# Kernel tuning notes

Hardware: AMD Instinct MI355X
Metric: run time of the kernel (lower is better)

Reference implementation:

```python
import jax, jax.numpy as jnp
import numpy as np

NUM_HEADS = 8

def mha(q, k, v, in_w, in_b, out_w, out_b):
    # q:[B,Lq,E] k,v:[B,Lk,E]; torch nn.MultiheadAttention math (batch_first)
    B, Lq, E = q.shape
    Lk = k.shape[1]
    H = NUM_HEADS
    D = E // H
    wq, wk, wv = in_w[:E], in_w[E:2*E], in_w[2*E:]      # each [E,E], torch layout [out,in]
    bq, bk, bv = in_b[:E], in_b[E:2*E], in_b[2*E:]
    qp = (q @ wq.T + bq).reshape(B, Lq, H, D)
    kp = (k @ wk.T + bk).reshape(B, Lk, H, D)
    vp = (v @ wv.T + bv).reshape(B, Lk, H, D)
    scores = jnp.einsum('bqhd,bkhd->bhqk', qp, kp) / jnp.sqrt(jnp.asarray(D, q.dtype))
    attn = jax.nn.softmax(scores, axis=-1)
    ctx = jnp.einsum('bhqk,bkhd->bqhd', attn, vp).reshape(B, Lq, E)
    return ctx @ out_w.T + out_b

def setup_inputs() -> dict:
    key = jax.random.key(0)
    ks = jax.random.split(key, 12)
    B, IN, E, M, NB = 2048, 1024, 512, 256, 8
    s = lambda *d: 1.0 / np.sqrt(d[-1])
    return {
        'x':      jax.random.normal(ks[0], (B, IN), jnp.float32),
        'memory': jax.random.uniform(ks[1], (M, E), jnp.float32, -s(E), s(E)),
        'enc_w':  jax.random.uniform(ks[2], (E, IN), jnp.float32, -s(IN), s(IN)),
        'enc_b':  jnp.zeros((E,), jnp.float32),
        'blk_w':  jax.random.uniform(ks[3], (NB, E, E), jnp.float32, -s(E), s(E)),
        'blk_b':  jnp.zeros((NB, E), jnp.float32),
        'in_w':   jax.random.uniform(ks[4], (3 * E, E), jnp.float32, -s(E), s(E)),
        'in_b':   jnp.zeros((3 * E,), jnp.float32),
        'out_w':  jax.random.uniform(ks[5], (E, E), jnp.float32, -s(E), s(E)),
        'out_b':  jnp.zeros((E,), jnp.float32),
        'dec_w':  jax.random.uniform(ks[6], (IN, E), jnp.float32, -s(E), s(E)),
        'dec_b':  jnp.zeros((IN,), jnp.float32),
    }

def reference(x, memory, enc_w, enc_b, blk_w, blk_b, in_w, in_b, out_w, out_b, dec_w, dec_b):
    B = x.shape[0]
    encoded = jnp.tanh(x @ enc_w.T + enc_b)                     # [B,E]
    # all block linears at once: [B, NB, E]
    memory_updates = jnp.einsum('be,noe->bno', encoded, blk_w) + blk_b
    mem = jnp.broadcast_to(memory[None], (B,) + memory.shape)   # [B,M,E]
    attended = mha(memory_updates, mem, mem, in_w, in_b, out_w, out_b)
    updated_memory = mem + jnp.mean(attended, axis=1, keepdims=True)
    retrieved = mha(encoded[:, None, :], updated_memory, updated_memory, in_w, in_b, out_w, out_b)
    output = retrieved[:, 0, :] @ dec_w.T + dec_b               # [B,IN]
    return output, updated_memory
```

## Files before the change

### kernel.cpp

```cpp
#include <hip/hip_runtime.h>
#include <math.h>


typedef __attribute__((ext_vector_type(8))) short short8;
typedef __attribute__((ext_vector_type(4))) float f32x4;
typedef unsigned short u16;

#define GLOAD16(gp, lp)                                                        \
    __builtin_amdgcn_global_load_lds(                                          \
        (const __attribute__((address_space(1))) void*)(gp),                   \
        (__attribute__((address_space(3))) void*)(lp), 16, 0, 0)

__device__ inline u16 bf16_rn(float x) {
    unsigned u = __float_as_uint(x);
    unsigned r = (u + 0x7FFFu + ((u >> 16) & 1u)) >> 16;
    return (u16)r;
}
__device__ inline float bf16_f(u16 h) { return __uint_as_float(((unsigned)h) << 16); }

__global__ __launch_bounds__(256)
void prep_all(const float* __restrict__ x, const float* __restrict__ mm,
              const float* __restrict__ ew, const float* __restrict__ iw,
              const float* __restrict__ ow, const float* __restrict__ dw,
              const float* __restrict__ blk_w,
              const float* __restrict__ in_b, const float* __restrict__ blk_b,
              const float* __restrict__ out_b, const float* __restrict__ dec_b,
              u16* __restrict__ xh, u16* __restrict__ xl,
              u16* __restrict__ mh, u16* __restrict__ ml,
              u16* __restrict__ ewh, u16* __restrict__ ewl,
              u16* __restrict__ iwh, u16* __restrict__ iwl,
              u16* __restrict__ owh, u16* __restrict__ owl,
              u16* __restrict__ dwh, u16* __restrict__ dwl,
              u16* __restrict__ bwTh, u16* __restrict__ bwTl,
              u16* __restrict__ owTh, u16* __restrict__ owTl,
              float* __restrict__ bias1, float* __restrict__ bias2,
              float* __restrict__ bias_uv)
{
    __shared__ float T[32][33];
    const int id = blockIdx.x;
    const int t = threadIdx.x;
    if (id < 2304) {
        const int z = id >> 8, within = id & 255;
        const float* s; u16 *dh, *dl;
        if (z < 8) { s = blk_w + (long long)z * 262144;
                     dh = bwTh + (long long)z * 262144; dl = bwTl + (long long)z * 262144; }
        else       { s = ow; dh = owTh; dl = owTl; }
        const int c0 = (within & 15) * 32, r0 = (within >> 4) * 32;
        const int tx = t & 31, ty = t >> 5;
        #pragma unroll
        for (int rr = 0; rr < 4; ++rr)
            T[ty + rr * 8][tx] = s[(long long)(r0 + ty + rr * 8) * 512 + c0 + tx];
        __syncthreads();
        #pragma unroll
        for (int rr = 0; rr < 4; ++rr) {
            float v = T[tx][ty + rr * 8];
            long long o = (long long)(c0 + ty + rr * 8) * 512 + r0 + tx;
            u16 hh = bf16_rn(v);
            dh[o] = hh; dl[o] = bf16_rn(v - bf16_f(hh));
        }
    } else if (id < 2326) {
        int idx = (id - 2304) * 256 + t;
        if (idx < 4096) {
            int n = idx >> 9, f = idx & 511;
            const float* wr_ = iw + (long long)f * 512;
            const float* bb  = blk_b + n * 512;
            float s = in_b[f];
            for (int o = 0; o < 512; ++o) s += wr_[o] * bb[o];
            bias1[idx] = s;
        } else if (idx < 5120) {
            int i = idx - 4096;
            const float* dr = dw + (long long)i * 512;
            float s = dec_b[i];
            for (int f = 0; f < 512; ++f) s += dr[f] * out_b[f];
            bias2[i] = s;
        } else if (idx < 5632) {
            int f = idx - 5120;
            const float* wv = iw + (long long)(1024 + f) * 512;
            float s = 0.f;
            for (int e = 0; e < 512; ++e) s += wv[e] * out_b[e];
            bias_uv[f] = s;
        }
    } else {
        const long long total = 1081344;
        const long long stride = 2048LL * 256;
        for (long long i = (long long)(id - 2326) * 256 + t; i < total; i += stride) {
            const float* src; u16 *hi, *lo; long long j;
            if (i < 524288)      { src = x;  hi = xh;  lo = xl;  j = i; }
            else if (i < 557056) { src = mm; hi = mh;  lo = ml;  j = i - 524288; }
            else if (i < 688128) { src = ew; hi = ewh; lo = ewl; j = i - 557056; }
            else if (i < 884736) { src = iw; hi = iwh; lo = iwl; j = i - 688128; }
            else if (i < 950272) { src = ow; hi = owh; lo = owl; j = i - 884736; }
            else                 { src = dw; hi = dwh; lo = dwl; j = i - 950272; }
            float4 v = reinterpret_cast<const float4*>(src)[j];
            u16 h0 = bf16_rn(v.x), h1 = bf16_rn(v.y), h2 = bf16_rn(v.z), h3 = bf16_rn(v.w);
            ushort4 hv = {h0, h1, h2, h3};
            ushort4 lv = {bf16_rn(v.x - bf16_f(h0)), bf16_rn(v.y - bf16_f(h1)),
                          bf16_rn(v.z - bf16_f(h2)), bf16_rn(v.w - bf16_f(h3))};
            reinterpret_cast<ushort4*>(hi)[j] = hv;
            reinterpret_cast<ushort4*>(lo)[j] = lv;
        }
    }
}

struct ZD {
    const u16 *Ah, *Al, *Bh, *Bl;
    const float* bias;
    float* Cf; u16 *Ch, *Cl;
    int M, lda, ldb, ldc, K, act, omode;
    float scale;
};
template<int NZ> struct ZPack { ZD d[NZ]; };

__device__ __forceinline__ void gemm_zd(const ZD& dz, int m0, int n0,
    u16 (*Ash)[32], u16 (*Asl)[32], u16 (*Bsh)[32], u16 (*Bsl)[32])
{
    const int t  = threadIdx.x;
    const int lane = t & 63;
    const int wid  = t >> 6;
    const int wr = (wid >> 1) * 64;
    const int wc = (wid & 1) * 32;
    const int lr = lane & 15;
    const int lk = (lane >> 4) << 3;

    f32x4 acc[4][2];
    const f32x4 zero = {0.f, 0.f, 0.f, 0.f};
    #pragma unroll
    for (int i = 0; i < 4; ++i)
        #pragma unroll
        for (int j = 0; j < 2; ++j) acc[i][j] = zero;

    const int sr = t >> 2;
    const int sc = (t & 3) << 3;
    char* AshB = (char*)&Ash[0][0];
    char* AslB = (char*)&Asl[0][0];
    char* BshB = (char*)&Bsh[0][0];
    char* BslB = (char*)&Bsl[0][0];
    const int wo = wid * 1024;

    const long long arow0 = (long long)(m0 + sr) * dz.lda + sc;
    const long long arow1 = (long long)(m0 + 64 + sr) * dz.lda + sc;
    const long long brow  = (long long)(n0 + sr) * dz.ldb + sc;

    for (int k0 = 0; k0 < dz.K; k0 += 32) {
        __syncthreads();
        GLOAD16(dz.Ah + arow0 + k0, AshB + wo);
        GLOAD16(dz.Ah + arow1 + k0, AshB + 4096 + wo);
        GLOAD16(dz.Al + arow0 + k0, AslB + wo);
        GLOAD16(dz.Al + arow1 + k0, AslB + 4096 + wo);
        GLOAD16(dz.Bh + brow  + k0, BshB + wo);
        GLOAD16(dz.Bl + brow  + k0, BslB + wo);
        __syncthreads();

        short8 fah[4], fal[4], fbh[2], fbl[2];
        #pragma unroll
        for (int i = 0; i < 4; ++i) {
            fah[i] = *reinterpret_cast<const short8*>(&Ash[wr + i * 16 + lr][lk]);
            fal[i] = *reinterpret_cast<const short8*>(&Asl[wr + i * 16 + lr][lk]);
        }
        #pragma unroll
        for (int j = 0; j < 2; ++j) {
            fbh[j] = *reinterpret_cast<const short8*>(&Bsh[wc + j * 16 + lr][lk]);
            fbl[j] = *reinterpret_cast<const short8*>(&Bsl[wc + j * 16 + lr][lk]);
        }
        #pragma unroll
        for (int i = 0; i < 4; ++i)
            #pragma unroll
            for (int j = 0; j < 2; ++j) {
                acc[i][j] = __builtin_amdgcn_mfma_f32_16x16x32_bf16(fah[i], fbh[j], acc[i][j], 0, 0, 0);
                acc[i][j] = __builtin_amdgcn_mfma_f32_16x16x32_bf16(fah[i], fbl[j], acc[i][j], 0, 0, 0);
                acc[i][j] = __builtin_amdgcn_mfma_f32_16x16x32_bf16(fal[i], fbh[j], acc[i][j], 0, 0, 0);
            }
    }

    #pragma unroll
    for (int j = 0; j < 2; ++j) {
        const int col = n0 + wc + j * 16 + lr;
        const float bv = dz.bias ? dz.bias[col] : 0.f;
        #pragma unroll
        for (int i = 0; i < 4; ++i) {
            #pragma unroll
            for (int q = 0; q < 4; ++q) {
                const int row = m0 + wr + i * 16 + ((lane >> 4) << 2) + q;
                float v = (acc[i][j][q] + bv) * dz.scale;
                if (dz.act) v = tanhf(v);
                if (dz.omode == 0) {
                    dz.Cf[(long long)row * dz.ldc + col] = v;
                } else {
                    long long off = (dz.omode == 1)
                        ? (long long)row * dz.ldc + col
                        : (long long)col * dz.ldc + row;
                    u16 h = bf16_rn(v);
                    dz.Ch[off] = h;
                    dz.Cl[off] = bf16_rn(v - bf16_f(h));
                }
            }
        }
    }
}

template<int NZ>
__global__ __launch_bounds__(256)
void gemm_multi(ZPack<NZ> pk)
{
    __shared__ u16 Ash[128][32];
    __shared__ u16 Asl[128][32];
    __shared__ u16 Bsh[64][32];
    __shared__ u16 Bsl[64][32];
    const ZD dz = pk.d[blockIdx.z];
    const int m0 = blockIdx.x * 128;
    if (m0 >= dz.M) return;
    gemm_zd(dz, m0, blockIdx.y * 64, Ash, Asl, Bsh, Bsl);
}

template<int MODE>
__device__ __forceinline__ void attn_body(char* smem, int bxblk, int h,
    const u16* __restrict__ Qph, const u16* __restrict__ Qpl,
    const u16* __restrict__ Kvh, const u16* __restrict__ Kvl,
    const u16* __restrict__ VTh, const u16* __restrict__ VTl,
    u16* __restrict__ Oh, u16* __restrict__ Ol)
{
    const int t = threadIdx.x;
    const int lane = t & 63, w = t >> 6;
    const int l15 = lane & 15, g = lane >> 4;
    const int wr = w * 32;
    const int b0 = bxblk * (MODE == 0 ? 16 : 128);

    u16* Qs = (u16*)smem;
    char* KsB = smem + 36864;

    for (int c = t; c < 2048; c += 256) {
        int plane = c >> 10, rem = c & 1023;
        int row = rem >> 3, seg = rem & 7;
        const u16* src = plane ? Qpl : Qph;
        long long addr;
        if (MODE == 0) {
            int q = row >> 4, bb = row & 15;
            addr = ((long long)q * 2048 + b0 + bb) * 512 + h * 64 + seg * 8;
        } else {
            addr = (long long)(b0 + row) * 512 + h * 64 + seg * 8;
        }
        *(int4*)(&Qs[plane * 9216 + row * 72 + seg * 8]) = *(const int4*)(src + addr);
    }

    f32x4 sacc[2][16];
    const f32x4 zero = {0.f, 0.f, 0.f, 0.f};
    #pragma unroll
    for (int i = 0; i < 2; ++i)
        #pragma unroll
        for (int j = 0; j < 16; ++j) sacc[i][j] = zero;

    short8 qfh[2][2], qfl[2][2];

    for (int kh = 0; kh < 2; ++kh) {
        if (kh) __syncthreads();
        for (int c = t; c < 2048; c += 256) {
            int plane = c >> 10, rem = c & 1023;
            int key = rem >> 3, seg = rem & 7;
            const u16* src = plane ? Kvl : Kvh;
            *(int4*)(KsB + plane * 18432 + key * 144 + seg * 16) =
                *(const int4*)(src + (long long)(kh * 128 + key) * 1024 + h * 64 + seg * 8);
        }
        __syncthreads();
        if (kh == 0) {
            #pragma unroll
            for (int i = 0; i < 2; ++i)
                #pragma unroll
                for (int kf = 0; kf < 2; ++kf) {
                    int ro = (wr + 16 * i + l15) * 72 + kf * 32 + g * 8;
                    qfh[i][kf] = *(const short8*)(&Qs[ro]);
                    qfl[i][kf] = *(const short8*)(&Qs[9216 + ro]);
                }
        }
        #pragma unroll
        for (int j = 0; j < 8; ++j) {
            int jg = kh * 8 + j;
            #pragma unroll
            for (int kf = 0; kf < 2; ++kf) {
                const char* kb = KsB + (j * 16 + l15) * 144 + (kf * 32 + g * 8) * 2;
                short8 kbh = *(const short8*)(kb);
                short8 kbl = *(const short8*)(kb + 18432);
                #pragma unroll
                for (int i = 0; i < 2; ++i) {
                    sacc[i][jg] = __builtin_amdgcn_mfma_f32_16x16x32_bf16(qfh[i][kf], kbh, sacc[i][jg], 0, 0, 0);
                    sacc[i][jg] = __builtin_amdgcn_mfma_f32_16x16x32_bf16(qfh[i][kf], kbl, sacc[i][jg], 0, 0, 0);
                    sacc[i][jg] = __builtin_amdgcn_mfma_f32_16x16x32_bf16(qfl[i][kf], kbh, sacc[i][jg], 0, 0, 0);
                }
            }
        }
    }

    float inv[2][4];
    #pragma unroll
    for (int i = 0; i < 2; ++i)
        #pragma unroll
        for (int q = 0; q < 4; ++q) {
            float m = -1e30f;
            #pragma unroll
            for (int j = 0; j < 16; ++j) m = fmaxf(m, sacc[i][j][q]);
            #pragma unroll
            for (int off = 1; off <= 8; off <<= 1) m = fmaxf(m, __shfl_xor(m, off, 64));
            #pragma unroll
            for (int j = 0; j < 16; ++j) sacc[i][j][q] = __expf(sacc[i][j][q] - m);
            float s = 0.f;
            #pragma unroll
            for (int j = 0; j < 16; ++j) s += sacc[i][j][q];
            #pragma unroll
            for (int off = 1; off <= 8; off <<= 1) s += __shfl_xor(s, off, 64);
            inv[i][q] = 1.0f / s;
        }

    f32x4 ctx[2][4];
    #pragma unroll
    for (int i = 0; i < 2; ++i)
        #pragma unroll
        for (int jd = 0; jd < 4; ++jd) ctx[i][jd] = zero;

    for (int qt = 0; qt < 4; ++qt) {
        __syncthreads();
        #pragma unroll
        for (int i = 0; i < 2; ++i)
            #pragma unroll
            for (int jj = 0; jj < 4; ++jj) {
                int jg = qt * 4 + jj;
                #pragma unroll
                for (int q = 0; q < 4; ++q) {
                    int row = wr + 16 * i + 4 * g + q;
                    int key = jj * 16 + l15;
                    float pv = sacc[i][jg][q];
                    u16 ph = bf16_rn(pv);
                    u16 pl = bf16_rn(pv - bf16_f(ph));
                    int byt = row * 128 + ((key * 2) ^ ((row & 7) << 4));
                    *(u16*)(smem + byt) = ph;
                    *(u16*)(smem + 16384 + byt) = pl;
                }
            }
        for (int c = t; c < 1024; c += 256) {
            int plane = c >> 9, rem = c & 511;
            int d = rem >> 3, seg = rem & 7;
            const u16* src = plane ? VTl : VTh;
            int4 v = *(const int4*)(src + (long long)h * 16384 + d * 256 + qt * 64 + seg * 8);
            int byt = 36864 + plane * 8192 + d * 128 + ((seg * 16) ^ ((d & 7) << 4));
            *(int4*)(smem + byt) = v;
        }
        __syncthreads();

        short8 pah[2][2], pal[2][2];
        #pragma unroll
        for (int i = 0; i < 2; ++i)
            #pragma unroll
            for (int kf = 0; kf < 2; ++kf) {
                int row = wr + 16 * i + l15;
                int byt = row * 128 + ((kf * 64 + g * 16) ^ ((row & 7) << 4));
                pah[i][kf] = *(const short8*)(smem + byt);
                pal[i][kf] = *(const short8*)(smem + 16384 + byt);
            }
        #pragma unroll
        for (int jd = 0; jd < 4; ++jd) {
            #pragma unroll
            for (int kf = 0; kf < 2; ++kf) {
                int d = 16 * jd + l15;
                int byt = 36864 + d * 128 + ((kf * 64 + g * 16) ^ ((d & 7) << 4));
                short8 vbh = *(const short8*)(smem + byt);
                short8 vbl = *(const short8*)(smem + 8192 + byt);
                #pragma unroll
                for (int i = 0; i < 2; ++i) {
                    ctx[i][jd] = __builtin_amdgcn_mfma_f32_16x16x32_bf16(pah[i][kf], vbh, ctx[i][jd], 0, 0, 0);
                    ctx[i][jd] = __builtin_amdgcn_mfma_f32_16x16x32_bf16(pah[i][kf], vbl, ctx[i][jd], 0, 0, 0);
                    ctx[i][jd] = __builtin_amdgcn_mfma_f32_16x16x32_bf16(pal[i][kf], vbh, ctx[i][jd], 0, 0, 0);
                }
            }
        }
    }

    if (MODE == 0) {
        __syncthreads();
        float* R = (float*)smem;
        #pragma unroll
        for (int i = 0; i < 2; ++i)
            #pragma unroll
            for (int jd = 0; jd < 4; ++jd)
                #pragma unroll
                for (int q = 0; q < 4; ++q) {
                    int qa = 2 * w + i;
                    int bb = 4 * g + q;
                    int d  = 16 * jd + l15;
                    R[qa * 1024 + bb * 64 + d] = ctx[i][jd][q] * inv[i][q];
                }
        __syncthreads();
        for (int o = t; o < 1024; o += 256) {
            int bb = o >> 6, d = o & 63;
            float s = 0.f;
            #pragma unroll
            for (int qa = 0; qa < 8; ++qa) s += R[qa * 1024 + bb * 64 + d];
            s *= 0.125f;
            long long addr = (long long)(b0 + bb) * 512 + h * 64 + d;
            u16 hh = bf16_rn(s);
            Oh[addr] = hh;
            Ol[addr] = bf16_rn(s - bf16_f(hh));
        }
    } else {
        #pragma unroll
        for (int i = 0; i < 2; ++i)
            #pragma unroll
            for (int jd = 0; jd < 4; ++jd)
                #pragma unroll
                for (int q = 0; q < 4; ++q) {
                    int b = b0 + wr + 16 * i + 4 * g + q;
                    int d = 16 * jd + l15;
                    long long addr = (long long)b * 1024 + h * 64 + d;
                    float v = ctx[i][jd][q] * inv[i][q];
                    u16 hh = bf16_rn(v);
                    Oh[addr] = hh;
                    Ol[addr] = bf16_rn(v - bf16_f(hh));
                }
    }
}

__global__ __launch_bounds__(256, 2)
void attn_both(const u16* __restrict__ Q1h, const u16* __restrict__ Q1l,
               const u16* __restrict__ Q2h, const u16* __restrict__ Q2l,
               const u16* __restrict__ Kvh, const u16* __restrict__ Kvl,
               const u16* __restrict__ VTh, const u16* __restrict__ VTl,
               u16* __restrict__ cbh, u16* __restrict__ cbl,
               u16* __restrict__ ach, u16* __restrict__ acl)
{
    extern __shared__ char smem[];
    const int id = blockIdx.x;
    if (id < 1024) {
        attn_body<0>(smem, id >> 3, id & 7, Q1h, Q1l, Kvh, Kvl, VTh, VTl,
                     cbh, cbl);
    } else {
        const int j = id - 1024;
        attn_body<1>(smem, j >> 3, j & 7, Q2h, Q2l, Kvh, Kvl, VTh, VTl,
                     ach, acl);
    }
}

__global__ __launch_bounds__(256)
void write_final(const u16* __restrict__ ach, const u16* __restrict__ acl,
                 const u16* __restrict__ bch, const u16* __restrict__ bcl,
                 const float* __restrict__ bias2, float* __restrict__ out,
                 const float* __restrict__ mem, const float* __restrict__ uf,
                 float* __restrict__ out1)
{
    __shared__ u16 Ash[128][32];
    __shared__ u16 Asl[128][32];
    __shared__ u16 Bsh[64][32];
    __shared__ u16 Bsl[64][32];
    const int id = blockIdx.x;
    if (id < 256) {
        ZD dz = { ach, acl, bch, bcl, bias2, out, nullptr, nullptr,
                  2048, 1024, 1024, 1024, 1024, 0, 0, 1.0f };
        gemm_zd(dz, (id & 15) * 128, (id >> 4) * 64, Ash, Asl, Bsh, Bsl);
    } else {
        const f32x4* m4 = reinterpret_cast<const f32x4*>(mem);
        const f32x4* u4 = reinterpret_cast<const f32x4*>(uf);
        f32x4* o4 = reinterpret_cast<f32x4*>(out1);
        long long i0 = (long long)(id - 256) * 16384 + threadIdx.x;
        #pragma unroll 4
        for (int j = 0; j < 64; ++j) {
            long long i = i0 + j * 256;
            int e4 = (int)(i & 127);
            int m  = (int)((i >> 7) & 255);
            long long b = i >> 15;
            f32x4 a = m4[m * 128 + e4];
            f32x4 c = u4[b * 128 + e4];
            f32x4 rr = a + c;
            __builtin_nontemporal_store(rr, &o4[i]);
        }
    }
}

extern "C" void kernel_launch(void* const* d_in, const int* in_sizes, int n_in,
                              void* d_out, int out_size, void* d_ws, size_t ws_size,
                              hipStream_t stream)
{
    (void)in_sizes; (void)n_in; (void)out_size; (void)ws_size;
    const float* x     = (const float*)d_in[0];
    const float* mem   = (const float*)d_in[1];
    const float* enc_w = (const float*)d_in[2];
    const float* enc_b = (const float*)d_in[3];
    const float* blk_w = (const float*)d_in[4];
    const float* blk_b = (const float*)d_in[5];
    const float* in_w  = (const float*)d_in[6];
    const float* in_b  = (const float*)d_in[7];
    const float* out_w = (const float*)d_in[8];
    const float* out_b = (const float*)d_in[9];
    const float* dec_w = (const float*)d_in[10];
    const float* dec_b = (const float*)d_in[11];
    float* out = (float*)d_out;

    char* p = (char*)d_ws;
    auto alloc = [&](size_t bytes) { char* q = p; p += (bytes + 255) & ~(size_t)255; return q; };
    u16* xh   = (u16*)alloc(2097152 * 2); u16* xl   = (u16*)alloc(2097152 * 2);
    u16* memh = (u16*)alloc(131072 * 2);  u16* meml = (u16*)alloc(131072 * 2);
    u16* ewh  = (u16*)alloc(524288 * 2);  u16* ewl  = (u16*)alloc(524288 * 2);
    u16* iwh  = (u16*)alloc(786432 * 2);  u16* iwl  = (u16*)alloc(786432 * 2);
    u16* owh  = (u16*)alloc(262144 * 2);  u16* owl  = (u16*)alloc(262144 * 2);
    u16* owTh = (u16*)alloc(262144 * 2);  u16* owTl = (u16*)alloc(262144 * 2);
    u16* dwh  = (u16*)alloc(524288 * 2);  u16* dwl  = (u16*)alloc(524288 * 2);
    u16* ench = (u16*)alloc(1048576 * 2); u16* encl = (u16*)alloc(1048576 * 2);
    u16* kvh  = (u16*)alloc(262144 * 2);  u16* kvl  = (u16*)alloc(262144 * 2);
    u16* vpTh = (u16*)alloc(131072 * 2);  u16* vpTl = (u16*)alloc(131072 * 2);
    float* bias1  = (float*)alloc(4096 * 4);
    float* bias2  = (float*)alloc(1024 * 4);
    float* biasuv = (float*)alloc(512 * 4);
    u16* cbh  = (u16*)alloc(1048576 * 2); u16* cbl  = (u16*)alloc(1048576 * 2);
    float* uf = (float*)alloc(1048576 * 4);
    u16* qp2h = (u16*)alloc(1048576 * 2); u16* qp2l = (u16*)alloc(1048576 * 2);
    u16* Wuvh = (u16*)alloc(262144 * 2);  u16* Wuvl = (u16*)alloc(262144 * 2);
    u16* ach  = (u16*)alloc(2097152 * 2); u16* acl  = (u16*)alloc(2097152 * 2);
    u16* bch  = (u16*)alloc(1048576 * 2); u16* bcl  = (u16*)alloc(1048576 * 2);

    float* out1 = out + 2097152;
    u16* bwTh = (u16*)out1;
    u16* bwTl = bwTh + 2097152;
    u16* W1h  = bwTl + 2097152;
    u16* W1l  = W1h + 2097152;
    u16* qp1h = W1l + 2097152;
    u16* qp1l = qp1h + 8388608;

    dim3 blk(256);

    prep_all<<<dim3(4374), blk, 0, stream>>>(x, mem, enc_w, in_w, out_w, dec_w,
        blk_w, in_b, blk_b, out_b, dec_b,
        xh, xl, memh, meml, ewh, ewl, iwh, iwl, owh, owl, dwh, dwl,
        bwTh, bwTl, owTh, owTl, bias1, bias2, biasuv);

    {
        ZPack<16> pk;
        pk.d[0] = { xh, xl, ewh, ewl, enc_b, nullptr, ench, encl,
                    2048, 1024, 1024, 512, 1024, 1, 1, 1.0f };
        for (int z = 0; z < 8; ++z)
            pk.d[1 + z] = { iwh, iwl, bwTh + (long long)z * 262144, bwTl + (long long)z * 262144,
                            nullptr, nullptr, W1h + (long long)z * 262144, W1l + (long long)z * 262144,
                            512, 512, 512, 512, 512, 0, 1, 1.0f };
        pk.d[9]  = { iwh + 1024 * 512, iwl + 1024 * 512, owTh, owTl, nullptr,
                     nullptr, Wuvh, Wuvl, 512, 512, 512, 512, 512, 0, 1, 1.0f };
        for (int s = 0; s < 2; ++s)
            for (int c = 0; c < 2; ++c)
                pk.d[10 + s * 2 + c] = { dwh + (long long)s * 262144, dwl + (long long)s * 262144,
                                         owTh, owTl, nullptr, nullptr,
                                         bch + (long long)s * 524288 + c * 512,
                                         bcl + (long long)s * 524288 + c * 512,
                                         512, 512, 512, 1024, 512, 0, 1, 1.0f };
        pk.d[14] = { memh, meml, iwh + 512 * 512, iwl + 512 * 512, in_b + 512,
                     nullptr, kvh, kvl, 256, 512, 512, 1024, 512, 0, 1, 1.0f };
        pk.d[15] = { memh, meml, iwh + 1024 * 512, iwl + 1024 * 512, in_b + 1024,
                     nullptr, vpTh, vpTl, 256, 512, 512, 256, 512, 0, 2, 1.0f };
        gemm_multi<16><<<dim3(16, 8, 16), blk, 0, stream>>>(pk);
    }
    {
        ZPack<9> pk;
        for (int z = 0; z < 8; ++z)
            pk.d[z] = { ench, encl, W1h + (long long)z * 262144, W1l + (long long)z * 262144,
                        bias1 + z * 512, nullptr,
                        qp1h + (long long)z * 1048576, qp1l + (long long)z * 1048576,
                        2048, 512, 512, 512, 512, 0, 1, 0.125f };
        pk.d[8] = { ench, encl, iwh, iwl, in_b, nullptr, qp2h, qp2l,
                    2048, 512, 512, 512, 512, 0, 1, 0.125f };
        gemm_multi<9><<<dim3(16, 8, 9), blk, 0, stream>>>(pk);
    }
    attn_both<<<dim3(1152), blk, 73728, stream>>>(qp1h, qp1l, qp2h, qp2l,
        kvh, kvl, vpTh, vpTl, cbh, cbl, ach, acl);
    {
        ZPack<2> pk;
        pk.d[0] = { cbh, cbl, owh, owl, out_b, uf, nullptr, nullptr,
                    2048, 512, 512, 512, 512, 0, 0, 1.0f };
        pk.d[1] = { cbh, cbl, Wuvh, Wuvl, biasuv, nullptr, ach + 512, acl + 512,
                    2048, 512, 512, 1024, 512, 0, 1, 1.0f };
        gemm_multi<2><<<dim3(16, 8, 2), blk, 0, stream>>>(pk);
    }
    write_final<<<dim3(4352), blk, 0, stream>>>(ach, acl, bch, bcl, bias2, out,
        mem, uf, out1);
}
```

Baseline: 487.7 us.

## Rebalance launches: move independent GEMMs and attn2 into co-scheduled kernels

Moves the independent weight-fold and decoder GEMMs out of the first batched GEMM launch and into the second, so the first launch holds only the encoder and W1 products and the second holds the Q projections plus those independent products. The second attention pass (128 blocks) is split from the first and runs in the same launch as the output-projection GEMMs (256 blocks), filling the tail of a small launch. The aim is better load balance and fewer underfilled waves. The cost is a heavier combined kernel whose large shared-memory request may reduce occupancy for the GEMM blocks.

```diff
diff --git a/kernel.cpp b/kernel.cpp
--- a/kernel.cpp
+++ b/kernel.cpp
@@ -417,22 +417,37 @@
 }
 
 __global__ __launch_bounds__(256, 2)
-void attn_both(const u16* __restrict__ Q1h, const u16* __restrict__ Q1l,
-               const u16* __restrict__ Q2h, const u16* __restrict__ Q2l,
-               const u16* __restrict__ Kvh, const u16* __restrict__ Kvl,
-               const u16* __restrict__ VTh, const u16* __restrict__ VTl,
-               u16* __restrict__ cbh, u16* __restrict__ cbl,
-               u16* __restrict__ ach, u16* __restrict__ acl)
+void attn1_k(const u16* __restrict__ Q1h, const u16* __restrict__ Q1l,
+             const u16* __restrict__ Kvh, const u16* __restrict__ Kvl,
+             const u16* __restrict__ VTh, const u16* __restrict__ VTl,
+             u16* __restrict__ cbh, u16* __restrict__ cbl)
+{
+    extern __shared__ char smem[];
+    attn_body<0>(smem, blockIdx.x >> 3, blockIdx.x & 7, Q1h, Q1l,
+                 Kvh, Kvl, VTh, VTl, cbh, cbl);
+}
+
+__global__ __launch_bounds__(256, 2)
+void attn2_u(const u16* __restrict__ Q2h, const u16* __restrict__ Q2l,
+             const u16* __restrict__ Kvh, const u16* __restrict__ Kvl,
+             const u16* __restrict__ VTh, const u16* __restrict__ VTl,
+             u16* __restrict__ ach, u16* __restrict__ acl,
+             ZPack<2> pk)
 {
     extern __shared__ char smem[];
     const int id = blockIdx.x;
-    if (id < 1024) {
-        attn_body<0>(smem, id >> 3, id & 7, Q1h, Q1l, Kvh, Kvl, VTh, VTl,
-                     cbh, cbl);
+    if (id < 128) {
+        attn_body<1>(smem, id >> 3, id & 7, Q2h, Q2l, Kvh, Kvl, VTh, VTl,
+                     ach, acl);
     } else {
-        const int j = id - 1024;
-        attn_body<1>(smem, j >> 3, j & 7, Q2h, Q2l, Kvh, Kvl, VTh, VTl,
-                     ach, acl);
+        const int gid = id - 128;
+        const ZD dz = pk.d[gid >> 7];
+        const int w = gid & 127;
+        gemm_zd(dz, (w & 15) * 128, (w >> 4) * 64,
+                (u16(*)[32])(smem),
+                (u16(*)[32])(smem + 8192),
+                (u16(*)[32])(smem + 16384),
+                (u16(*)[32])(smem + 20480));
     }
 }
 
@@ -528,13 +543,24 @@
         bwTh, bwTl, owTh, owTl, bias1, bias2, biasuv);
 
     {
-        ZPack<16> pk;
+        ZPack<9> pk;
         pk.d[0] = { xh, xl, ewh, ewl, enc_b, nullptr, ench, encl,
                     2048, 1024, 1024, 512, 1024, 1, 1, 1.0f };
         for (int z = 0; z < 8; ++z)
             pk.d[1 + z] = { iwh, iwl, bwTh + (long long)z * 262144, bwTl + (long long)z * 262144,
                             nullptr, nullptr, W1h + (long long)z * 262144, W1l + (long long)z * 262144,
                             512, 512, 512, 512, 512, 0, 1, 1.0f };
+        gemm_multi<9><<<dim3(16, 8, 9), blk, 0, stream>>>(pk);
+    }
+    {
+        ZPack<16> pk;
+        for (int z = 0; z < 8; ++z)
+            pk.d[z] = { ench, encl, W1h + (long long)z * 262144, W1l + (long long)z * 262144,
+                        bias1 + z * 512, nullptr,
+                        qp1h + (long long)z * 1048576, qp1l + (long long)z * 1048576,
+                        2048, 512, 512, 512, 512, 0, 1, 0.125f };
+        pk.d[8] = { ench, encl, iwh, iwl, in_b, nullptr, qp2h, qp2l,
+                    2048, 512, 512, 512, 512, 0, 1, 0.125f };
         pk.d[9]  = { iwh + 1024 * 512, iwl + 1024 * 512, owTh, owTl, nullptr,
                      nullptr, Wuvh, Wuvl, 512, 512, 512, 512, 512, 0, 1, 1.0f };
         for (int s = 0; s < 2; ++s)
@@ -550,26 +576,16 @@
                      nullptr, vpTh, vpTl, 256, 512, 512, 256, 512, 0, 2, 1.0f };
         gemm_multi<16><<<dim3(16, 8, 16), blk, 0, stream>>>(pk);
     }
-    {
-        ZPack<9> pk;
-        for (int z = 0; z < 8; ++z)
-            pk.d[z] = { ench, encl, W1h + (long long)z * 262144, W1l + (long long)z * 262144,
-                        bias1 + z * 512, nullptr,
-                        qp1h + (long long)z * 1048576, qp1l + (long long)z * 1048576,
-                        2048, 512, 512, 512, 512, 0, 1, 0.125f };
-        pk.d[8] = { ench, encl, iwh, iwl, in_b, nullptr, qp2h, qp2l,
-                    2048, 512, 512, 512, 512, 0, 1, 0.125f };
-        gemm_multi<9><<<dim3(16, 8, 9), blk, 0, stream>>>(pk);
-    }
-    attn_both<<<dim3(1152), blk, 73728, stream>>>(qp1h, qp1l, qp2h, qp2l,
-        kvh, kvl, vpTh, vpTl, cbh, cbl, ach, acl);
+    attn1_k<<<dim3(1024), blk, 73728, stream>>>(qp1h, qp1l, kvh, kvl,
+        vpTh, vpTl, cbh, cbl);
     {
         ZPack<2> pk;
         pk.d[0] = { cbh, cbl, owh, owl, out_b, uf, nullptr, nullptr,
                     2048, 512, 512, 512, 512, 0, 0, 1.0f };
         pk.d[1] = { cbh, cbl, Wuvh, Wuvl, biasuv, nullptr, ach + 512, acl + 512,
                     2048, 512, 512, 1024, 512, 0, 1, 1.0f };
-        gemm_multi<2><<<dim3(16, 8, 2), blk, 0, stream>>>(pk);
+        attn2_u<<<dim3(384), blk, 73728, stream>>>(qp2h, qp2l, kvh, kvl,
+            vpTh, vpTl, ach, acl, pk);
     }
     write_final<<<dim3(4352), blk, 0, stream>>>(ach, acl, bch, bcl, bias2, out,
         mem, uf, out1);
```

Measured after the change: 473.0 us (median of 2 runs). 3.0% less time.
